# Performance work log

Hardware: AMD Instinct MI355X
Metric: run time of the kernel (lower is better)

Reference implementation:

```python
import jax, jax.numpy as jnp
import numpy as np

BETA = 0.25
EPS = 1e-10


def setup_inputs() -> dict:
    key = jax.random.key(0)
    k1, k2 = jax.random.split(key)
    x = jax.random.normal(k1, (32, 64, 64, 64), dtype=jnp.float32)  # [B, C=embed_dim, H, W]
    embeddings = jax.random.normal(k2, (64, 512), dtype=jnp.float32)  # [embed_dim, K]
    return {"x": x, "embeddings": embeddings}


def reference(x, embeddings):
    B, C, H, W = x.shape
    K = embeddings.shape[1]
    sg = jax.lax.stop_gradient

    z_e = jnp.transpose(x, (0, 2, 3, 1))          # [B, H, W, C]
    z_flat = z_e.reshape(-1, C)                    # [N, C]

    # Squared L2 distances to codebook: ||z||^2 + ||e||^2 - 2 z.e
    dists = (
        jnp.sum(z_flat * z_flat, axis=1, keepdims=True)
        + jnp.sum(embeddings * embeddings, axis=0)
        - 2.0 * (z_flat @ embeddings)
    )                                              # [N, K]
    idx = jnp.argmin(dists, axis=1)                # [N]

    # Direct gather instead of one-hot matmul (same math)
    quantized = embeddings.T[idx].reshape(z_e.shape)  # [B, H, W, C]

    e_latent_loss = jnp.mean((sg(quantized) - z_e) ** 2)
    q_latent_loss = jnp.mean((quantized - sg(z_e)) ** 2)
    loss = q_latent_loss + BETA * e_latent_loss

    # Straight-through estimator
    quantized_st = z_e + sg(quantized - z_e)

    # Perplexity via codebook usage histogram (== mean of one-hot encodings)
    N = idx.shape[0]
    counts = jnp.zeros((K,), dtype=jnp.float32).at[idx].add(1.0)
    avg_probs = counts / N
    perplexity = jnp.exp(-jnp.sum(avg_probs * jnp.log(avg_probs + EPS)))

    quantized_out = jnp.transpose(quantized_st, (0, 3, 1, 2))  # [B, C, H, W]
    encoding_indices = idx.reshape(B, H, W)
    return loss, quantized_out, perplexity, encoding_indices
```

## Files before the change

kernel.cpp:

```cpp
#include <hip/hip_runtime.h>


#define B_ 32
#define C_ 64
#define HW_ 4096
#define K_ 512
#define N_ (B_ * HW_)
#define NC_ ((long long)N_ * C_)
#define ROWS_ 64
#define NBLK_ (N_ / ROWS_)
#define NSLOT_ 8

typedef __attribute__((ext_vector_type(8))) short short8;
typedef __attribute__((ext_vector_type(4))) float float4_t;


__device__ __forceinline__ unsigned short f2bf(float f) {
    unsigned u = __float_as_uint(f);
    u += 0x7fffu + ((u >> 16) & 1u);
    return (unsigned short)(u >> 16);
}
__device__ __forceinline__ float bf2f(unsigned short h) {
    return __uint_as_float(((unsigned)h) << 16);
}
__device__ __forceinline__ void merge2(float& m1, int& i1, float& m2,
                                       float om1, int oi1, float om2) {
    if (om1 < m1) { m2 = fminf(m1, om2); m1 = om1; i1 = oi1; }
    else          { m2 = fminf(m2, om1); }
}

__global__ __launch_bounds__(512) void vq_init(const float* __restrict__ emb,
                                               float* __restrict__ snmax_p,
                                               float* __restrict__ en,
                                               float* __restrict__ embT32,
                                               unsigned short* __restrict__ fBhi,
                                               unsigned short* __restrict__ fBlo,
                                               int* __restrict__ ghist8) {
    __shared__ float smax[8];
    int k = threadIdx.x;
    if (blockIdx.x < 64) {
        int c = blockIdx.x;
        float e = emb[c * K_ + k];
        embT32[k * C_ + c] = e;
        float s = -2.0f * e;
        unsigned short hi = f2bf(s);
        unsigned short lo = f2bf(s - bf2f(hi));
        int kk   = c >> 5;
        int lane = (((c & 31) >> 3) << 4) + (k & 15);
        int fb   = ((k >> 5) << 2) + (((k >> 4) & 1) << 1) + kk;
        int off  = (fb << 9) + (lane << 3) + (c & 7);
        fBhi[off] = hi;
        fBlo[off] = lo;
    } else {
#pragma unroll
        for (int s8 = 0; s8 < NSLOT_; ++s8) ghist8[(s8 << 9) + k] = 0;
        float s = 0.f;
#pragma unroll
        for (int c = 0; c < C_; ++c) {
            float e = emb[c * K_ + k];
            s += e * e;
        }
        en[k] = s;
        float m = s;
#pragma unroll
        for (int off = 32; off > 0; off >>= 1)
            m = fmaxf(m, __shfl_down(m, off, 64));
        if ((k & 63) == 0) smax[k >> 6] = m;
        __syncthreads();
        if (k == 0) {
            float mm = smax[0];
#pragma unroll
            for (int w2 = 1; w2 < 8; ++w2) mm = fmaxf(mm, smax[w2]);
            *snmax_p = 4.0f * mm;
        }
    }
}

__global__ __launch_bounds__(256) void vq_argmin(const float* __restrict__ x,
                                                 const float* __restrict__ en_g,
                                                 const float* __restrict__ embT32,
                                                 const unsigned short* __restrict__ fBhi,
                                                 const unsigned short* __restrict__ fBlo,
                                                 const float* __restrict__ snmax_p,
                                                 float* __restrict__ out_q,
                                                 float* __restrict__ out_idx,
                                                 int* __restrict__ ghist8,
                                                 double* __restrict__ ssepart) {
    __shared__ float sEn[K_];
    __shared__ float znrow[ROWS_];
    __shared__ int   biarr[ROWS_];
    __shared__ int   flaglist[ROWS_];
    __shared__ float wsse[4];
    __shared__ int   nflag;

    const int t    = threadIdx.x;
    const int lane = t & 63;
    const int w    = t >> 6;
    const int ln15 = lane & 15;
    const int quad = lane >> 4;
    const int n0   = blockIdx.x * ROWS_;
    const int b    = n0 >> 12;
    const int hw0  = n0 & 4095;
    const float* xbase = x + ((size_t)b << 18) + hw0;
    const int myrow = (w << 4) + ln15;

    if (t == 0) nflag = 0;
    sEn[t]       = en_g[t];
    sEn[256 + t] = en_g[256 + t];

    float v0[8], v1[8];
#pragma unroll
    for (int j = 0; j < 8; ++j) {
        v0[j] = xbase[((size_t)((quad << 3) + j) << 12) + myrow];
        v1[j] = xbase[((size_t)(32 + (quad << 3) + j) << 12) + myrow];
    }
    short8 ah0, al0, ah1, al1;
    float znacc = 0.f;
#pragma unroll
    for (int j = 0; j < 8; ++j) {
        unsigned short h0 = f2bf(v0[j]);
        ah0[j] = (short)h0;
        al0[j] = (short)f2bf(v0[j] - bf2f(h0));
        unsigned short h1 = f2bf(v1[j]);
        ah1[j] = (short)h1;
        al1[j] = (short)f2bf(v1[j] - bf2f(h1));
        znacc += v0[j] * v0[j] + v1[j] * v1[j];
    }
    znacc += __shfl_xor(znacc, 16, 64);
    znacc += __shfl_xor(znacc, 32, 64);
    if (quad == 0) znrow[myrow] = znacc;
    __syncthreads();

    const float snm = *snmax_p;

    float m1[4], m2[4];
    int   i1[4];
#pragma unroll
    for (int reg = 0; reg < 4; ++reg) {
        m1[reg] = 3.4e38f; m2[reg] = 3.4e38f; i1[reg] = 0;
    }

    for (int p = 0; p < 16; ++p) {
#pragma unroll
        for (int ct = 0; ct < 2; ++ct) {
            const int cbase = (p << 5) + (ct << 4);
            const int fbase = ((((p << 2) + (ct << 1)) << 9) + (lane << 3));
            short8 bh0 = *(const short8*)(fBhi + fbase);
            short8 bh1 = *(const short8*)(fBhi + fbase + 512);
            short8 bl0 = *(const short8*)(fBlo + fbase);
            short8 bl1 = *(const short8*)(fBlo + fbase + 512);
            float env = sEn[cbase + ln15];
            int   idx = cbase + ln15;
            float4_t a0 = {env, env, env, env};
            float4_t a1 = {0.f, 0.f, 0.f, 0.f};
            a0 = __builtin_amdgcn_mfma_f32_16x16x32_bf16(al0, bh0, a0, 0, 0, 0);
            a1 = __builtin_amdgcn_mfma_f32_16x16x32_bf16(al1, bh1, a1, 0, 0, 0);
            a0 = __builtin_amdgcn_mfma_f32_16x16x32_bf16(ah0, bl0, a0, 0, 0, 0);
            a1 = __builtin_amdgcn_mfma_f32_16x16x32_bf16(ah1, bl1, a1, 0, 0, 0);
            a0 = __builtin_amdgcn_mfma_f32_16x16x32_bf16(ah0, bh0, a0, 0, 0, 0);
            a1 = __builtin_amdgcn_mfma_f32_16x16x32_bf16(ah1, bh1, a1, 0, 0, 0);
#pragma unroll
            for (int reg = 0; reg < 4; ++reg) {
                float vv = a0[reg] + a1[reg];
                bool  lt = vv < m1[reg];
                float mx = fmaxf(vv, m1[reg]);
                m2[reg] = fminf(m2[reg], mx);
                m1[reg] = fminf(m1[reg], vv);
                i1[reg] = lt ? idx : i1[reg];
            }
        }
    }

#pragma unroll
    for (int reg = 0; reg < 4; ++reg) {
        float a1v = m1[reg], a2v = m2[reg];
        int   ai  = i1[reg];
#pragma unroll
        for (int s = 1; s < 16; s <<= 1) {
            float o1 = __shfl_xor(a1v, s, 16);
            int   oi = __shfl_xor(ai, s, 16);
            float o2 = __shfl_xor(a2v, s, 16);
            merge2(a1v, ai, a2v, o1, oi, o2);
        }
        if (ln15 == 0) {
            int row = (w << 4) + (quad << 2) + reg;
            float znr = znrow[row];
            float W = 1.4e-4f * __builtin_sqrtf(znr * snm) + 1e-3f;
            biarr[row] = ai;
            if (a2v > a1v + W) {
                out_idx[n0 + row] = (float)ai;
            } else {
                int pos = atomicAdd(&nflag, 1);
                flaglist[pos] = row;
            }
        }
    }
    __syncthreads();

    int nf = nflag;
    for (int f = w; f < nf; f += 4) {
        int r = flaglist[f];
        float zl = xbase[((size_t)lane << 12) + r];
        float d[8];
#pragma unroll
        for (int j = 0; j < 8; ++j) d[j] = 0.f;
        for (int c4 = 0; c4 < 16; ++c4) {
            float z0 = __shfl(zl, (c4 << 2) + 0, 64);
            float z1 = __shfl(zl, (c4 << 2) + 1, 64);
            float z2 = __shfl(zl, (c4 << 2) + 2, 64);
            float z3 = __shfl(zl, (c4 << 2) + 3, 64);
#pragma unroll
            for (int j = 0; j < 8; ++j) {
                float4_t e = *(const float4_t*)(embT32 + ((((lane << 3) + j) << 6) + (c4 << 2)));
                d[j] = fmaf(z0, e[0], d[j]);
                d[j] = fmaf(z1, e[1], d[j]);
                d[j] = fmaf(z2, e[2], d[j]);
                d[j] = fmaf(z3, e[3], d[j]);
            }
        }
        float znr = znrow[r];
        float best = 3.4e38f;
        int   bidx = 0;
#pragma unroll
        for (int j = 0; j < 8; ++j) {
            int k = (lane << 3) + j;
            float dist = (znr + sEn[k]) - 2.f * d[j];
            if (dist < best) { best = dist; bidx = k; }
        }
#pragma unroll
        for (int off = 32; off > 0; off >>= 1) {
            float ov = __shfl_down(best, off, 64);
            int   oi = __shfl_down(bidx, off, 64);
            if (ov < best || (ov == best && oi < bidx)) { best = ov; bidx = oi; }
        }
        if (lane == 0) {
            biarr[r] = bidx;
            out_idx[n0 + r] = (float)bidx;
        }
    }
    __syncthreads();

    const int code  = biarr[myrow];
    const float* eb = embT32 + (code << 6) + (quad << 3);
    float4_t e0 = *(const float4_t*)(eb);
    float4_t e1 = *(const float4_t*)(eb + 4);
    float4_t e2 = *(const float4_t*)(eb + 32);
    float4_t e3 = *(const float4_t*)(eb + 36);
    float* qrow = out_q + ((size_t)b << 18) + hw0 + myrow;
    float sacc = 0.f;
#pragma unroll
    for (int j = 0; j < 4; ++j) {
        int c0 = (quad << 3) + j;
        int c1 = (quad << 3) + 4 + j;
        float zA = bf2f((unsigned short)ah0[j])     + bf2f((unsigned short)al0[j]);
        float zB = bf2f((unsigned short)ah0[4 + j]) + bf2f((unsigned short)al0[4 + j]);
        float dA = e0[j] - zA, dB = e1[j] - zB;
        sacc += dA * dA + dB * dB;
        qrow[(size_t)c0 << 12] = e0[j];
        qrow[(size_t)c1 << 12] = e1[j];
        float zC = bf2f((unsigned short)ah1[j])     + bf2f((unsigned short)al1[j]);
        float zD = bf2f((unsigned short)ah1[4 + j]) + bf2f((unsigned short)al1[4 + j]);
        float dC = e2[j] - zC, dD = e3[j] - zD;
        sacc += dC * dC + dD * dD;
        qrow[(size_t)(32 + c0) << 12] = e2[j];
        qrow[(size_t)(32 + c1) << 12] = e3[j];
    }
#pragma unroll
    for (int off = 32; off > 0; off >>= 1)
        sacc += __shfl_down(sacc, off, 64);
    if (lane == 0) wsse[w] = sacc;
    __syncthreads();

    if (t == 0)
        ssepart[blockIdx.x] = (double)wsse[0] + (double)wsse[1]
                            + (double)wsse[2] + (double)wsse[3];
    if (t < ROWS_)
        __hip_atomic_fetch_add(&ghist8[((blockIdx.x & (NSLOT_ - 1)) << 9) + biarr[t]],
                               1, __ATOMIC_RELAXED, __HIP_MEMORY_SCOPE_AGENT);
}

__global__ __launch_bounds__(512) void vq_final(const int* __restrict__ ghist8,
                                                const double* __restrict__ ssepart,
                                                float* __restrict__ out_loss,
                                                float* __restrict__ out_perp) {
    __shared__ float  wsf[8];
    __shared__ double wsd[8];
    int t = threadIdx.x;
    int hsum = 0;
#pragma unroll
    for (int s8 = 0; s8 < NSLOT_; ++s8)
        hsum += ghist8[(s8 << 9) + t];
    float p = (float)hsum / (float)N_;
    float s = p * logf(p + 1e-10f);
    double d = ssepart[t] + ssepart[t + 512] + ssepart[t + 1024] + ssepart[t + 1536];
#pragma unroll
    for (int off = 32; off > 0; off >>= 1) {
        s += __shfl_down(s, off, 64);
        d += __shfl_down(d, off, 64);
    }
    if ((t & 63) == 0) { wsf[t >> 6] = s; wsd[t >> 6] = d; }
    __syncthreads();
    if (t == 0) {
        float  S = 0.f;
        double D = 0.0;
#pragma unroll
        for (int w = 0; w < 8; ++w) { S += wsf[w]; D += wsd[w]; }
        *out_perp = expf(-S);
        *out_loss = (float)(1.25 * D / (double)NC_);
    }
}

extern "C" void kernel_launch(void* const* d_in, const int* in_sizes, int n_in,
                              void* d_out, int out_size, void* d_ws, size_t ws_size,
                              hipStream_t stream) {
    const float* x   = (const float*)d_in[0];
    const float* emb = (const float*)d_in[1];

    float* out      = (float*)d_out;
    float* out_loss = out;
    float* out_q    = out + 1;
    float* out_perp = out + 1 + (size_t)N_ * C_;
    float* out_idx  = out + 2 + (size_t)N_ * C_;

    char* ws = (char*)d_ws;
    float*          snmax_p  = (float*)(ws + 56);
    float*          en       = (float*)(ws + 2112);
    float*          embT32   = (float*)(ws + 4160);
    unsigned short* fBhi     = (unsigned short*)(ws + 135232);
    unsigned short* fBlo     = (unsigned short*)(ws + 200768);
    int*            ghist8   = (int*)(ws + 266304);
    double*         ssepart  = (double*)(ws + 282688);

    vq_init<<<65, 512, 0, stream>>>(emb, snmax_p, en, embT32, fBhi, fBlo, ghist8);
    vq_argmin<<<NBLK_, 256, 0, stream>>>(x, en, embT32, fBhi, fBlo, snmax_p,
                                         out_q, out_idx, ghist8, ssepart);
    vq_final<<<1, 512, 0, stream>>>(ghist8, ssepart, out_loss, out_perp);
}
```

Baseline: 164.7 us.

## Stage codebook fragments through double-buffered LDS with async global-to-LDS loads

Each of the four waves used to fetch the same bf16 hi/lo codebook fragments straight from global memory. Now each 32-code chunk is loaded once per block into a double-buffered LDS area with global_load_lds. Every wave reads it from LDS, and the next-but-one chunk is prefetched after a block barrier. The goal is to cut redundant global/L2 traffic and hide load latency behind the MFMA work. The cost is a __syncthreads every iteration, 16 KB of extra LDS, and a launch-bounds occupancy hint. Correctness depends on the async LDS writes being complete before they are read.

Measured after the change: 196.3 us. 19.2% more time.

```diff
diff --git a/kernel.cpp b/kernel.cpp
--- a/kernel.cpp
+++ b/kernel.cpp
@@ -76,7 +76,69 @@
     }
 }
 
-__global__ __launch_bounds__(256) void vq_argmin(const float* __restrict__ x,
+#define STAGE(bufi, pp) do {                                                   \
+    int eoff_ = ((pp) << 11) + (w << 9) + (lane << 3);                         \
+    __builtin_amdgcn_global_load_lds(                                          \
+        (const __attribute__((address_space(1))) unsigned*)(fBhi + eoff_),     \
+        (__attribute__((address_space(3))) unsigned*)&LB[bufi][0][(w << 9)],   \
+        16, 0, 0);                                                             \
+    __builtin_amdgcn_global_load_lds(                                          \
+        (const __attribute__((address_space(1))) unsigned*)(fBlo + eoff_),     \
+        (__attribute__((address_space(3))) unsigned*)&LB[bufi][1][(w << 9)],   \
+        16, 0, 0);                                                             \
+} while (0)
+
+#define COMP_LDS(bufi, pp) do {                                                \
+    const unsigned short* hb_ = &LB[bufi][0][lane << 3];                       \
+    const unsigned short* lb_ = &LB[bufi][1][lane << 3];                       \
+    short8 h0_ = *(const short8*)(hb_);                                        \
+    short8 h1_ = *(const short8*)(hb_ + 512);                                  \
+    short8 g0_ = *(const short8*)(hb_ + 1024);                                 \
+    short8 g1_ = *(const short8*)(hb_ + 1536);                                 \
+    short8 l0_ = *(const short8*)(lb_);                                        \
+    short8 l1_ = *(const short8*)(lb_ + 512);                                  \
+    short8 q0_ = *(const short8*)(lb_ + 1024);                                 \
+    short8 q1_ = *(const short8*)(lb_ + 1536);                                 \
+    const int cb_ = ((pp) << 5) + ln15;                                        \
+    float env0_ = sEn[cb_];                                                    \
+    float env1_ = sEn[cb_ + 16];                                               \
+    float4_t a0 = {env0_, env0_, env0_, env0_};                                \
+    float4_t a1 = {0.f, 0.f, 0.f, 0.f};                                        \
+    float4_t b0 = {env1_, env1_, env1_, env1_};                                \
+    float4_t b1 = {0.f, 0.f, 0.f, 0.f};                                        \
+    a0 = __builtin_amdgcn_mfma_f32_16x16x32_bf16(al0, h0_, a0, 0, 0, 0);       \
+    a1 = __builtin_amdgcn_mfma_f32_16x16x32_bf16(al1, h1_, a1, 0, 0, 0);       \
+    b0 = __builtin_amdgcn_mfma_f32_16x16x32_bf16(al0, g0_, b0, 0, 0, 0);       \
+    b1 = __builtin_amdgcn_mfma_f32_16x16x32_bf16(al1, g1_, b1, 0, 0, 0);       \
+    a0 = __builtin_amdgcn_mfma_f32_16x16x32_bf16(ah0, l0_, a0, 0, 0, 0);       \
+    a1 = __builtin_amdgcn_mfma_f32_16x16x32_bf16(ah1, l1_, a1, 0, 0, 0);       \
+    b0 = __builtin_amdgcn_mfma_f32_16x16x32_bf16(ah0, q0_, b0, 0, 0, 0);       \
+    b1 = __builtin_amdgcn_mfma_f32_16x16x32_bf16(ah1, q1_, b1, 0, 0, 0);       \
+    a0 = __builtin_amdgcn_mfma_f32_16x16x32_bf16(ah0, h0_, a0, 0, 0, 0);       \
+    a1 = __builtin_amdgcn_mfma_f32_16x16x32_bf16(ah1, h1_, a1, 0, 0, 0);       \
+    b0 = __builtin_amdgcn_mfma_f32_16x16x32_bf16(ah0, g0_, b0, 0, 0, 0);       \
+    b1 = __builtin_amdgcn_mfma_f32_16x16x32_bf16(ah1, g1_, b1, 0, 0, 0);       \
+    _Pragma("unroll")                                                          \
+    for (int reg = 0; reg < 4; ++reg) {                                        \
+        float vv = a0[reg] + a1[reg];                                          \
+        bool  lt = vv < m1[reg];                                               \
+        float mx = fmaxf(vv, m1[reg]);                                         \
+        m2[reg] = fminf(m2[reg], mx);                                          \
+        m1[reg] = fminf(m1[reg], vv);                                          \
+        i1[reg] = lt ? cb_ : i1[reg];                                          \
+    }                                                                          \
+    _Pragma("unroll")                                                          \
+    for (int reg = 0; reg < 4; ++reg) {                                        \
+        float vv = b0[reg] + b1[reg];                                          \
+        bool  lt = vv < m1[reg];                                               \
+        float mx = fmaxf(vv, m1[reg]);                                         \
+        m2[reg] = fminf(m2[reg], mx);                                          \
+        m1[reg] = fminf(m1[reg], vv);                                          \
+        i1[reg] = lt ? (cb_ + 16) : i1[reg];                                   \
+    }                                                                          \
+} while (0)
+
+__global__ __launch_bounds__(256, 6) void vq_argmin(const float* __restrict__ x,
                                                  const float* __restrict__ en_g,
                                                  const float* __restrict__ embT32,
                                                  const unsigned short* __restrict__ fBhi,
@@ -86,6 +148,7 @@
                                                  float* __restrict__ out_idx,
                                                  int* __restrict__ ghist8,
                                                  double* __restrict__ ssepart) {
+    __shared__ unsigned short LB[2][2][2048];
     __shared__ float sEn[K_];
     __shared__ float znrow[ROWS_];
     __shared__ int   biarr[ROWS_];
@@ -108,6 +171,9 @@
     sEn[t]       = en_g[t];
     sEn[256 + t] = en_g[256 + t];
 
+    STAGE(0, 0);
+    STAGE(1, 1);
+
     float v0[8], v1[8];
 #pragma unroll
     for (int j = 0; j < 8; ++j) {
@@ -140,35 +206,12 @@
         m1[reg] = 3.4e38f; m2[reg] = 3.4e38f; i1[reg] = 0;
     }
 
+#pragma unroll 2
     for (int p = 0; p < 16; ++p) {
-#pragma unroll
-        for (int ct = 0; ct < 2; ++ct) {
-            const int cbase = (p << 5) + (ct << 4);
-            const int fbase = ((((p << 2) + (ct << 1)) << 9) + (lane << 3));
-            short8 bh0 = *(const short8*)(fBhi + fbase);
-            short8 bh1 = *(const short8*)(fBhi + fbase + 512);
-            short8 bl0 = *(const short8*)(fBlo + fbase);
-            short8 bl1 = *(const short8*)(fBlo + fbase + 512);
-            float env = sEn[cbase + ln15];
-            int   idx = cbase + ln15;
-            float4_t a0 = {env, env, env, env};
-            float4_t a1 = {0.f, 0.f, 0.f, 0.f};
-            a0 = __builtin_amdgcn_mfma_f32_16x16x32_bf16(al0, bh0, a0, 0, 0, 0);
-            a1 = __builtin_amdgcn_mfma_f32_16x16x32_bf16(al1, bh1, a1, 0, 0, 0);
-            a0 = __builtin_amdgcn_mfma_f32_16x16x32_bf16(ah0, bl0, a0, 0, 0, 0);
-            a1 = __builtin_amdgcn_mfma_f32_16x16x32_bf16(ah1, bl1, a1, 0, 0, 0);
-            a0 = __builtin_amdgcn_mfma_f32_16x16x32_bf16(ah0, bh0, a0, 0, 0, 0);
-            a1 = __builtin_amdgcn_mfma_f32_16x16x32_bf16(ah1, bh1, a1, 0, 0, 0);
-#pragma unroll
-            for (int reg = 0; reg < 4; ++reg) {
-                float vv = a0[reg] + a1[reg];
-                bool  lt = vv < m1[reg];
-                float mx = fmaxf(vv, m1[reg]);
-                m2[reg] = fminf(m2[reg], mx);
-                m1[reg] = fminf(m1[reg], vv);
-                i1[reg] = lt ? idx : i1[reg];
-            }
-        }
+        const int bufi = p & 1;
+        COMP_LDS(bufi, p);
+        __syncthreads();
+        if (p < 14) STAGE(bufi, p + 2);
     }
 
 #pragma unroll
```
